# Kernel optimization log

Measured on AMD Instinct MI355X. Metric: run time of the kernel, lower is better.

Reference implementation:

```python
import jax, jax.numpy as jnp
import numpy as np

N_EMBD = 1024
N_HEAD = 16
HEAD_DIM = N_EMBD // N_HEAD


def setup_inputs() -> dict:
    key = jax.random.key(0)
    ks = jax.random.split(key, 5)
    B, S = 2, 2048
    scale = 0.02
    return {
        "hidden_states": jax.random.normal(ks[0], (B, S, N_EMBD), dtype=jnp.float32),
        "w_attn": jax.random.normal(ks[1], (N_EMBD, 3 * N_EMBD), dtype=jnp.float32) * scale,
        "b_attn": jnp.zeros((3 * N_EMBD,), dtype=jnp.float32),
        "w_proj": jax.random.normal(ks[2], (N_EMBD, N_EMBD), dtype=jnp.float32) * scale,
        "b_proj": jnp.zeros((N_EMBD,), dtype=jnp.float32),
    }


def reference(hidden_states, w_attn, b_attn, w_proj, b_proj):
    B, S, _ = hidden_states.shape
    qkv = hidden_states @ w_attn + b_attn                     # [B,S,3E]
    q, k, v = jnp.split(qkv, 3, axis=-1)                      # each [B,S,E]

    def split_heads(t):  # [B,S,E] -> [B,H,S,D]
        return t.reshape(B, S, N_HEAD, HEAD_DIM).transpose(0, 2, 1, 3)

    q, k, v = split_heads(q), split_heads(k), split_heads(v)

    scores = jnp.einsum("bhqd,bhkd->bhqk", q, k) / np.sqrt(HEAD_DIM).astype(np.float32)
    causal = jnp.tril(jnp.ones((S, S), dtype=bool))
    scores = jnp.where(causal[None, None], scores, jnp.float32(-jnp.inf))
    attn = jax.nn.softmax(scores, axis=-1)                    # [B,H,S,S]
    out = jnp.einsum("bhqk,bhkd->bhqd", attn, v)              # [B,H,S,D]
    out = out.transpose(0, 2, 1, 3).reshape(B, S, N_EMBD)     # merge heads
    out = out @ w_proj + b_proj
    return out
```

## Files before the change

kernel.cpp:

```cpp
#include <hip/hip_runtime.h>
#include <hip/hip_bf16.h>


typedef __attribute__((ext_vector_type(4))) float  float4v;
typedef __attribute__((ext_vector_type(8))) short  short8v;
typedef __attribute__((ext_vector_type(4))) short  short4v;

#define ATT_SCALE 0.18033688011112042f

__device__ __forceinline__ short f2bf(float f) {
  union { float f; unsigned u; } v; v.f = f;
  unsigned r = v.u + 0x7fffu + ((v.u >> 16) & 1u);
  return (short)(r >> 16);
}
__device__ __forceinline__ float bf2f(short s) {
  union { unsigned u; float f; } v; v.u = ((unsigned)(unsigned short)s) << 16;
  return v.f;
}

__device__ __forceinline__ short4v pack_bf16x4(float a, float b, float c, float d) {
  unsigned x0 = __builtin_bit_cast(unsigned, a) + 0x8000u;
  unsigned x1 = __builtin_bit_cast(unsigned, b) + 0x8000u;
  unsigned x2 = __builtin_bit_cast(unsigned, c) + 0x8000u;
  unsigned x3 = __builtin_bit_cast(unsigned, d) + 0x8000u;
  union { unsigned u[2]; short4v s; } r;
  r.u[0] = __builtin_amdgcn_perm(x1, x0, 0x07060302);
  r.u[1] = __builtin_amdgcn_perm(x3, x2, 0x07060302);
  return r.s;
}

__device__ __forceinline__ void gl_lds16(const void* g, void* l) {
  __builtin_amdgcn_global_load_lds(
      (const __attribute__((address_space(1))) unsigned*)g,
      (__attribute__((address_space(3))) unsigned*)l, 16, 0, 0);
}

__global__ __launch_bounds__(256) void prep_kernel(
    const float* __restrict__ hidden, const float* __restrict__ w_attn,
    const float* __restrict__ w_proj, short* __restrict__ hA,
    short* __restrict__ wqkvT, short* __restrict__ wprojT) {
  __shared__ float tile[32][33];
  const int bx = blockIdx.x, t = threadIdx.x;
  if (bx < 4096) {
    const size_t i = ((size_t)bx * 256 + t) * 4;
    float4v v = *(const float4v*)(hidden + i);
    short4v o;
    #pragma unroll
    for (int k = 0; k < 4; k++) o[k] = f2bf(v[k]);
    *(short4v*)(hA + i) = o;
    return;
  }
  const float* in; short* out; int R, C, cx, cy;
  if (bx < 4096 + 3072) {
    in = w_attn; out = wqkvT; R = 1024; C = 3072;
    cx = (bx - 4096) % 96; cy = (bx - 4096) / 96;
  } else {
    in = w_proj; out = wprojT; R = 1024; C = 1024;
    cx = (bx - 7168) % 32; cy = (bx - 7168) / 32;
  }
  const int tx = t & 31, ty = t >> 5;
  const int c0 = cx * 32, r0 = cy * 32;
  #pragma unroll
  for (int i = 0; i < 4; i++)
    tile[ty + i * 8][tx] = in[(size_t)(r0 + ty + i * 8) * C + c0 + tx];
  __syncthreads();
  #pragma unroll
  for (int i = 0; i < 4; i++) {
    const int cc = ty + i * 8;
    out[(size_t)(c0 + cc) * R + r0 + tx] = f2bf(tile[tx][cc]);
  }
}

template<int RB, int MODE>
__global__ __launch_bounds__(256) void gemm_bt(
    const short* __restrict__ A, const short* __restrict__ Bt,
    const float* __restrict__ bias, void* __restrict__ Cout,
    short* __restrict__ vA, int M, int N, int K)
{
  __shared__ short As[2][RB][32];
  __shared__ short Bs[2][128][32];
  const int MI = RB / 32;
  const int t    = threadIdx.x;
  const int lane = t & 63;
  const int wave = t >> 6;
  const int wm   = (wave >> 1) * (RB / 2);
  const int wn   = (wave & 1) * 64;
  const int l16  = lane & 15;
  const int quad = lane >> 4;
  const int row0 = blockIdx.y * RB;
  const int col0 = blockIdx.x * 128;

  float4v acc[MI][4] = {};

  const int srow = lane >> 2;
  const int scol = (lane & 3) * 8;
  const int gcol = ((lane & 3) ^ ((srow >> 1) & 3)) * 8;
  const int rquad = (quad ^ ((l16 >> 1) & 3)) * 8;

  const short* gA0 = A + (size_t)(row0 + wave * ((RB == 128) ? 32 : 16) + srow) * K + gcol;
  const short* gA1 = gA0 + (size_t)16 * K;
  const short* gB0 = Bt + (size_t)(col0 + wave * 32 + srow) * K + gcol;
  const short* gB1 = gB0 + (size_t)16 * K;

  const int NI = K / 32;
  {
    if (RB == 128) {
      gl_lds16(gA0, &As[0][wave * 32 + srow][scol]);
      gl_lds16(gA1, &As[0][wave * 32 + 16 + srow][scol]);
    } else {
      gl_lds16(gA0, &As[0][(wave * 16 + srow) & (RB - 1)][scol]);
    }
    gl_lds16(gB0, &Bs[0][wave * 32 + srow][scol]);
    gl_lds16(gB1, &Bs[0][wave * 32 + 16 + srow][scol]);
  }

  for (int i = 0; i < NI; i++) {
    const int buf = i & 1;
    __syncthreads();
    if (i + 1 < NI) {
      const int k1 = (i + 1) * 32;
      if (RB == 128) {
        gl_lds16(gA0 + k1, &As[buf ^ 1][wave * 32 + srow][scol]);
        gl_lds16(gA1 + k1, &As[buf ^ 1][wave * 32 + 16 + srow][scol]);
      } else {
        gl_lds16(gA0 + k1, &As[buf ^ 1][(wave * 16 + srow) & (RB - 1)][scol]);
      }
      gl_lds16(gB0 + k1, &Bs[buf ^ 1][wave * 32 + srow][scol]);
      gl_lds16(gB1 + k1, &Bs[buf ^ 1][wave * 32 + 16 + srow][scol]);
    }
    short8v af[MI], bf[4];
    #pragma unroll
    for (int ii = 0; ii < MI; ii++)
      af[ii] = *(const short8v*)&As[buf][wm + ii * 16 + l16][rquad];
    #pragma unroll
    for (int j = 0; j < 4; j++)
      bf[j] = *(const short8v*)&Bs[buf][wn + j * 16 + l16][rquad];
    #pragma unroll
    for (int ii = 0; ii < MI; ii++)
      #pragma unroll
      for (int j = 0; j < 4; j++)
        acc[ii][j] = __builtin_amdgcn_mfma_f32_16x16x32_bf16(af[ii], bf[j], acc[ii][j], 0, 0, 0);
  }

  if (MODE == 2 && col0 >= 2048) {
    const int b  = row0 >> 11;
    const int hh = ((col0 - 2048) >> 6) + (wn >> 6);
    const int kt = ((row0 & 2047) >> 6) + (wm >> 6);
    short* vbase = vA + ((size_t)((b * 16 + hh) * 32 + kt) * 8) * 512;
    #pragma unroll
    for (int j = 0; j < 4; j++) {
      const float bv = bias[col0 + wn + j * 16 + l16];
      #pragma unroll
      for (int kwp = 0; kwp < 2; kwp++) {
        short8v s8;
        #pragma unroll
        for (int kw = 0; kw < 2; kw++) {
          short4v q4 = pack_bf16x4(acc[kwp * 2 + kw][j][0] + bv,
                                   acc[kwp * 2 + kw][j][1] + bv,
                                   acc[kwp * 2 + kw][j][2] + bv,
                                   acc[kwp * 2 + kw][j][3] + bv);
          #pragma unroll
          for (int r = 0; r < 4; r++) s8[kw * 4 + r] = q4[r];
        }
        *(short8v*)(vbase + ((size_t)(kwp * 4 + j) * 64 + lane) * 8) = s8;
      }
    }
    return;
  }

  #pragma unroll
  for (int j = 0; j < 4; j++) {
    const int col = col0 + wn + j * 16 + l16;
    const float sc = (MODE == 2 && col < 1024) ? ATT_SCALE : 1.0f;
    const float bv = bias[col];
    #pragma unroll
    for (int i = 0; i < MI; i++) {
      #pragma unroll
      for (int r = 0; r < 4; r++) {
        const int row = row0 + wm + i * 16 + quad * 4 + r;
        const float v = (acc[i][j][r] + bv) * sc;
        if (MODE == 2) ((short*)Cout)[(size_t)row * N + col] = f2bf(v);
        else           ((float*)Cout)[(size_t)row * N + col] = v;
      }
    }
  }
}

__global__ __launch_bounds__(256, 2) void attn_mfma(
    const short* __restrict__ qkv, const short* __restrict__ vA,
    short* __restrict__ P0, short* __restrict__ P1, float* __restrict__ lp)
{
  __shared__ short KA[2][8 * 512];
  __shared__ short VA[2][8 * 512];

  const int bh = blockIdx.y;
  const int b = bh >> 4, h = bh & 15;
  const int s = blockIdx.x;
  int qt = 0, sbase = 0;
  for (;;) { const int nc = (qt >> 3) + 1; if (s < sbase + nc) break; sbase += nc; qt++; }
  const int c = s - sbase;
  const int kt0  = c * 8;
  const int kend = min(qt + 1, kt0 + 8);

  const int t = threadIdx.x;
  const int lane = t & 63, w = t >> 6;
  const int l16 = lane & 15, quad = lane >> 4;

  const size_t base = (size_t)b * 2048 * 3072;
  const int qoff = h * 64, koff = 1024 + h * 64;
  const int qg = qt * 64 + w * 16 + l16;

  short8v qf[2];
  #pragma unroll
  for (int ks = 0; ks < 2; ks++)
    qf[ks] = *(const short8v*)(qkv + base + (size_t)qg * 3072 + qoff + ks * 32 + quad * 8);

  float4v O[4] = {};
  float l = 0.0f;

  const int id0 = w * 2, id1 = id0 + 1;
  const int jm0 = id0 & 3, ks0 = id0 >> 2;
  const int jm1 = id1 & 3, ks1 = id1 >> 2;
  const short* kg0 = qkv + base + (size_t)(jm0 * 16 + l16) * 3072 + koff + ks0 * 32 + quad * 8;
  const short* kg1 = qkv + base + (size_t)(jm1 * 16 + l16) * 3072 + koff + ks1 * 32 + quad * 8;
  const short* vg  = vA + (size_t)(bh * 32) * 4096 + lane * 8;

  gl_lds16(kg0 + (size_t)kt0 * 64 * 3072, &KA[0][id0 * 512 + lane * 8]);
  gl_lds16(kg1 + (size_t)kt0 * 64 * 3072, &KA[0][id1 * 512 + lane * 8]);
  gl_lds16(vg + (size_t)kt0 * 4096 + id0 * 512, &VA[0][id0 * 512 + lane * 8]);
  gl_lds16(vg + (size_t)kt0 * 4096 + id1 * 512, &VA[0][id1 * 512 + lane * 8]);

  for (int kt = kt0; kt < kend; kt++) {
    const int buf = (kt - kt0) & 1;
    __syncthreads();
    if (kt + 1 < kend) {
      gl_lds16(kg0 + (size_t)(kt + 1) * 64 * 3072, &KA[buf ^ 1][id0 * 512 + lane * 8]);
      gl_lds16(kg1 + (size_t)(kt + 1) * 64 * 3072, &KA[buf ^ 1][id1 * 512 + lane * 8]);
      gl_lds16(vg + (size_t)(kt + 1) * 4096 + id0 * 512, &VA[buf ^ 1][id0 * 512 + lane * 8]);
      gl_lds16(vg + (size_t)(kt + 1) * 4096 + id1 * 512, &VA[buf ^ 1][id1 * 512 + lane * 8]);
    }

    float4v sv[4] = {};
    #pragma unroll
    for (int ks = 0; ks < 2; ks++)
      #pragma unroll
      for (int jm = 0; jm < 4; jm++) {
        const short8v kf = *(const short8v*)&KA[buf][(ks * 4 + jm) * 512 + lane * 8];
        sv[jm] = __builtin_amdgcn_mfma_f32_16x16x32_bf16(kf, qf[ks], sv[jm], 0, 0, 0);
      }

    if (kt == qt) {
      #pragma unroll
      for (int jm = 0; jm < 4; jm++) {
        const int kv = kt * 64 + jm * 16 + quad * 4;
        #pragma unroll
        for (int r = 0; r < 4; r++)
          if (kv + r > qg) sv[jm][r] = -INFINITY;
      }
    }

    short4v pk[4];
    #pragma unroll
    for (int jm = 0; jm < 4; jm++) {
      float p0 = exp2f(sv[jm][0]), p1 = exp2f(sv[jm][1]);
      float p2 = exp2f(sv[jm][2]), p3 = exp2f(sv[jm][3]);
      l += (p0 + p1) + (p2 + p3);
      pk[jm] = pack_bf16x4(p0, p1, p2, p3);
    }

    #pragma unroll
    for (int id = 0; id < 8; id++) {
      const int kwp = id >> 2, dm = id & 3;
      const short8v vv = *(const short8v*)&VA[buf][id * 512 + lane * 8];
      const short4v v0 = {vv[0], vv[1], vv[2], vv[3]};
      const short4v v1 = {vv[4], vv[5], vv[6], vv[7]};
      O[dm] = __builtin_amdgcn_mfma_f32_16x16x16bf16_1k(v0, pk[kwp * 2],     O[dm], 0, 0, 0);
      O[dm] = __builtin_amdgcn_mfma_f32_16x16x16bf16_1k(v1, pk[kwp * 2 + 1], O[dm], 0, 0, 0);
    }
  }

  l += __shfl_xor(l, 16);
  l += __shfl_xor(l, 32);
  const int i = bh * 80 + s;
  short* pp = (i < 2048) ? (P0 + (size_t)i * 4096) : (P1 + (size_t)(i - 2048) * 4096);
  const int row = w * 16 + l16;
  if (quad == 0) lp[(size_t)i * 64 + row] = l;
  short* pr = pp + row * 64;
  #pragma unroll
  for (int dm = 0; dm < 4; dm++)
    *(short4v*)(pr + dm * 16 + quad * 4) =
        pack_bf16x4(O[dm][0], O[dm][1], O[dm][2], O[dm][3]);
}

__global__ __launch_bounds__(256) void merge_attn(
    const short* __restrict__ P0, const short* __restrict__ P1,
    const float* __restrict__ lp, short* __restrict__ aout)
{
  const int idx = blockIdx.x * 256 + threadIdx.x;
  const int q = idx >> 7;
  const int rest = idx & 127;
  const int h  = rest >> 3;
  const int dg = (rest & 7) * 8;
  const int b  = q >> 11;
  const int qr = q & 2047;
  const int qt = qr >> 6;
  const int row = qr & 63;
  const int a = qt >> 3, bq = qt & 7;
  const int off = qt + 4 * a * (a - 1) + a * bq;
  const int nc  = a + 1;
  const int bh  = b * 16 + h;

  float acc[8] = {};
  float suml = 0.0f;
  for (int c = 0; c < nc; c++) {
    const int i = bh * 80 + off + c;
    const short* pp = (i < 2048) ? (P0 + (size_t)i * 4096) : (P1 + (size_t)(i - 2048) * 4096);
    const short8v o = *(const short8v*)(pp + row * 64 + dg);
    #pragma unroll
    for (int k = 0; k < 8; k++) acc[k] += bf2f(o[k]);
    suml += lp[(size_t)i * 64 + row];
  }
  const float inv = 1.0f / suml;
  short8v ov;
  #pragma unroll
  for (int k = 0; k < 8; k++) ov[k] = f2bf(acc[k] * inv);
  *(short8v*)(aout + (size_t)q * 1024 + h * 64 + dg) = ov;
}

extern "C" void kernel_launch(void* const* d_in, const int* in_sizes, int n_in,
                              void* d_out, int out_size, void* d_ws, size_t ws_size,
                              hipStream_t stream) {
  const float* hidden = (const float*)d_in[0];
  const float* w_attn = (const float*)d_in[1];
  const float* b_attn = (const float*)d_in[2];
  const float* w_proj = (const float*)d_in[3];
  const float* b_proj = (const float*)d_in[4];
  float* outp = (float*)d_out;

  char* ws = (char*)d_ws;
  short* hA     = (short*)(ws);
  float* lp     = (float*)(ws + 8ull  * 1024 * 1024);
  short* wqkvT  = (short*)(ws + 8ull  * 1024 * 1024);
  short* wprojT = (short*)(ws + 14ull * 1024 * 1024);
  short* qkvb   = (short*)(ws + 16ull * 1024 * 1024);
  short* vAbuf  = (short*)(ws + 40ull * 1024 * 1024);
  short* aout   = (short*)(ws + 40ull * 1024 * 1024);
  short* P0     = (short*)d_out;

  prep_kernel<<<8192, 256, 0, stream>>>(hidden, w_attn, w_proj, hA, wqkvT, wprojT);
  gemm_bt<128, 2><<<dim3(24, 32), 256, 0, stream>>>(hA, wqkvT, b_attn, qkvb, vAbuf, 4096, 3072, 1024);
  attn_mfma<<<dim3(80, 32), 256, 0, stream>>>(qkvb, vAbuf, P0, hA, lp);
  merge_attn<<<2048, 256, 0, stream>>>(P0, hA, lp, aout);
  gemm_bt<64, 0><<<dim3(8, 64), 256, 0, stream>>>(aout, wprojT, b_proj, outp, nullptr, 4096, 1024, 1024);
}
```

Baseline: 202.5 us.

## Load V directly to registers, reverse block order, add setprio and fast exp/cvt

The attention kernel stops staging V through LDS and has each lane load its eight V fragments straight from global memory into registers at the start of every key tile. It also reverses the block index so the longest query tiles are scheduled first, wraps the MFMA sections in s_setprio, and switches to the raw exp2 builtin and the hardware v_cvt_pk_bf16_f32 packing instruction. The aim is to cut LDS traffic and instruction count and to improve load balance. In exchange, V loads are no longer prefetched a tile ahead, which can expose global latency, and register pressure goes up.

```diff
diff --git a/kernel.cpp b/kernel.cpp
--- a/kernel.cpp
+++ b/kernel.cpp
@@ -26,6 +26,13 @@
   union { unsigned u[2]; short4v s; } r;
   r.u[0] = __builtin_amdgcn_perm(x1, x0, 0x07060302);
   r.u[1] = __builtin_amdgcn_perm(x3, x2, 0x07060302);
+  return r.s;
+}
+
+__device__ __forceinline__ short4v cvt_pk_bf16x4(float a, float b, float c, float d) {
+  union { unsigned u[2]; short4v s; } r;
+  asm("v_cvt_pk_bf16_f32 %0, %1, %2" : "=v"(r.u[0]) : "v"(a), "v"(b));
+  asm("v_cvt_pk_bf16_f32 %0, %1, %2" : "=v"(r.u[1]) : "v"(c), "v"(d));
   return r.s;
 }
 
@@ -191,11 +198,10 @@
     short* __restrict__ P0, short* __restrict__ P1, float* __restrict__ lp)
 {
   __shared__ short KA[2][8 * 512];
-  __shared__ short VA[2][8 * 512];
 
   const int bh = blockIdx.y;
   const int b = bh >> 4, h = bh & 15;
-  const int s = blockIdx.x;
+  const int s = 79 - blockIdx.x;
   int qt = 0, sbase = 0;
   for (;;) { const int nc = (qt >> 3) + 1; if (s < sbase + nc) break; sbase += nc; qt++; }
   const int c = s - sbase;
@@ -227,20 +233,23 @@
 
   gl_lds16(kg0 + (size_t)kt0 * 64 * 3072, &KA[0][id0 * 512 + lane * 8]);
   gl_lds16(kg1 + (size_t)kt0 * 64 * 3072, &KA[0][id1 * 512 + lane * 8]);
-  gl_lds16(vg + (size_t)kt0 * 4096 + id0 * 512, &VA[0][id0 * 512 + lane * 8]);
-  gl_lds16(vg + (size_t)kt0 * 4096 + id1 * 512, &VA[0][id1 * 512 + lane * 8]);
 
   for (int kt = kt0; kt < kend; kt++) {
     const int buf = (kt - kt0) & 1;
     __syncthreads();
+
+    short8v vv[8];
+    #pragma unroll
+    for (int id = 0; id < 8; id++)
+      vv[id] = *(const short8v*)(vg + (size_t)kt * 4096 + id * 512);
+
     if (kt + 1 < kend) {
       gl_lds16(kg0 + (size_t)(kt + 1) * 64 * 3072, &KA[buf ^ 1][id0 * 512 + lane * 8]);
       gl_lds16(kg1 + (size_t)(kt + 1) * 64 * 3072, &KA[buf ^ 1][id1 * 512 + lane * 8]);
-      gl_lds16(vg + (size_t)(kt + 1) * 4096 + id0 * 512, &VA[buf ^ 1][id0 * 512 + lane * 8]);
-      gl_lds16(vg + (size_t)(kt + 1) * 4096 + id1 * 512, &VA[buf ^ 1][id1 * 512 + lane * 8]);
     }
 
     float4v sv[4] = {};
+    __builtin_amdgcn_s_setprio(1);
     #pragma unroll
     for (int ks = 0; ks < 2; ks++)
       #pragma unroll
@@ -248,6 +257,7 @@
         const short8v kf = *(const short8v*)&KA[buf][(ks * 4 + jm) * 512 + lane * 8];
         sv[jm] = __builtin_amdgcn_mfma_f32_16x16x32_bf16(kf, qf[ks], sv[jm], 0, 0, 0);
       }
+    __builtin_amdgcn_s_setprio(0);
 
     if (kt == qt) {
       #pragma unroll
@@ -262,21 +272,25 @@
     short4v pk[4];
     #pragma unroll
     for (int jm = 0; jm < 4; jm++) {
-      float p0 = exp2f(sv[jm][0]), p1 = exp2f(sv[jm][1]);
-      float p2 = exp2f(sv[jm][2]), p3 = exp2f(sv[jm][3]);
+      float p0 = __builtin_amdgcn_exp2f(sv[jm][0]);
+      float p1 = __builtin_amdgcn_exp2f(sv[jm][1]);
+      float p2 = __builtin_amdgcn_exp2f(sv[jm][2]);
+      float p3 = __builtin_amdgcn_exp2f(sv[jm][3]);
       l += (p0 + p1) + (p2 + p3);
-      pk[jm] = pack_bf16x4(p0, p1, p2, p3);
-    }
-
+      pk[jm] = cvt_pk_bf16x4(p0, p1, p2, p3);
+    }
+
+    __builtin_amdgcn_s_setprio(1);
     #pragma unroll
     for (int id = 0; id < 8; id++) {
       const int kwp = id >> 2, dm = id & 3;
-      const short8v vv = *(const short8v*)&VA[buf][id * 512 + lane * 8];
-      const short4v v0 = {vv[0], vv[1], vv[2], vv[3]};
-      const short4v v1 = {vv[4], vv[5], vv[6], vv[7]};
+      const short8v v8 = vv[id];
+      const short4v v0 = {v8[0], v8[1], v8[2], v8[3]};
+      const short4v v1 = {v8[4], v8[5], v8[6], v8[7]};
       O[dm] = __builtin_amdgcn_mfma_f32_16x16x16bf16_1k(v0, pk[kwp * 2],     O[dm], 0, 0, 0);
       O[dm] = __builtin_amdgcn_mfma_f32_16x16x16bf16_1k(v1, pk[kwp * 2 + 1], O[dm], 0, 0, 0);
     }
+    __builtin_amdgcn_s_setprio(0);
   }
 
   l += __shfl_xor(l, 16);
```

Measured after the change: 203.7 us. Within noise of the previous version (+0.6%).
